# Optimization experiments

Hardware: AMD Instinct MI355X
Metric: run time of the kernel (lower is better)

## Reference

```python
import jax, jax.numpy as jnp
import numpy as np

IMG = 1024.0
NMS_THRESH = 0.7
PRE_NMS_TOPK = 1000
POST_NMS_TOPK = 1000
MIN_BOX_SIZE = 0.0
SCALE_CLAMP = float(np.log(1000.0 / 16.0))
NEG = -1e9
LVL_OFFSET = 2.0 * IMG  # batched_nms coordinate-offset trick: boxes from different levels never overlap

_STRIDES = [4, 8, 16, 32, 64]
_SIZES = [32.0, 64.0, 128.0, 256.0, 512.0]
_RATIOS = [0.5, 1.0, 2.0]


def _make_anchors():
    """Detectron2 DefaultAnchorGenerator anchors (offset=0)."""
    out = []
    for s, size in zip(_STRIDES, _SIZES):
        area = size * size
        base = []
        for r in _RATIOS:
            w = np.sqrt(area / r)
            h = r * w
            base.append([-w / 2.0, -h / 2.0, w / 2.0, h / 2.0])
        base = np.asarray(base, np.float32)  # [A,4]
        H = int(IMG) // s
        coords = np.arange(H, dtype=np.float32) * s
        sx, sy = np.meshgrid(coords, coords)
        shifts = np.stack([sx.ravel(), sy.ravel(), sx.ravel(), sy.ravel()], axis=1)  # [HW,4]
        anchors = (shifts[:, None, :] + base[None, :, :]).reshape(-1, 4).astype(np.float32)
        out.append(jnp.asarray(anchors))
    return out


def setup_inputs() -> dict:
    key = jax.random.key(0)
    N = 4
    names = ["p2", "p3", "p4", "p5", "p6"]
    anchors = _make_anchors()
    inp = {}
    for i, (nm, an) in enumerate(zip(names, anchors)):
        HWA = an.shape[0]
        k1 = jax.random.fold_in(key, 2 * i)
        k2 = jax.random.fold_in(key, 2 * i + 1)
        inp[f"logits_{nm}"] = jax.random.normal(k1, (N, HWA), jnp.float32)
        # small deltas so decoded proposals stay realistic
        inp[f"deltas_{nm}"] = 0.1 * jax.random.normal(k2, (N, HWA, 4), jnp.float32)
        inp[f"anchors_{nm}"] = an
    return inp


def _apply_deltas(deltas, anchors):
    """Box2BoxTransform.apply_deltas with weights (1,1,1,1)."""
    wa = anchors[..., 2] - anchors[..., 0]
    ha = anchors[..., 3] - anchors[..., 1]
    cxa = anchors[..., 0] + 0.5 * wa
    cya = anchors[..., 1] + 0.5 * ha
    dx, dy, dw, dh = (deltas[..., i] for i in range(4))
    dw = jnp.minimum(dw, SCALE_CLAMP)
    dh = jnp.minimum(dh, SCALE_CLAMP)
    cx = dx * wa + cxa
    cy = dy * ha + cya
    w = wa * jnp.exp(dw)
    h = ha * jnp.exp(dh)
    return jnp.stack([cx - 0.5 * w, cy - 0.5 * h, cx + 0.5 * w, cy + 0.5 * h], axis=-1)


def _pairwise_iou(b):
    area = (b[:, 2] - b[:, 0]) * (b[:, 3] - b[:, 1])
    lt = jnp.maximum(b[:, None, :2], b[None, :, :2])
    rb = jnp.minimum(b[:, None, 2:], b[None, :, 2:])
    wh = jnp.clip(rb - lt, 0.0)
    inter = wh[..., 0] * wh[..., 1]
    return inter / (area[:, None] + area[None, :] - inter + 1e-9)


def _nms_single(boxes, scores, lvl):
    """Greedy batched NMS (per-level via coordinate offset) + post-NMS top-k. boxes [M,4]."""
    M = boxes.shape[0]
    order = jnp.argsort(-scores)
    boxes = boxes[order]
    scores = scores[order]
    lvl = lvl[order]
    off_boxes = boxes + (lvl.astype(boxes.dtype) * LVL_OFFSET)[:, None]
    iou = _pairwise_iou(off_boxes)  # [M,M]
    valid = scores > NEG / 2
    idx = jnp.arange(M)

    def body(supp, xs):
        row, i, v = xs
        keep_i = (~supp[i]) & v
        supp = supp | (keep_i & (row > NMS_THRESH) & (idx > i))
        return supp, None

    supp, _ = jax.lax.scan(body, jnp.zeros((M,), bool), (iou, idx, valid))
    kept_scores = jnp.where((~supp) & valid, scores, NEG)
    top_s, top_i = jax.lax.top_k(kept_scores, POST_NMS_TOPK)
    return boxes[top_i], top_s


def _forward(logits_list, deltas_list, anchors_list):
    all_b, all_s, all_l = [], [], []
    for li, (lg, dl, an) in enumerate(zip(logits_list, deltas_list, anchors_list)):
        props = _apply_deltas(dl, an[None, :, :])  # [N,HWA,4]
        k = min(PRE_NMS_TOPK, lg.shape[1])
        sc, idx = jax.lax.top_k(lg, k)  # per-level pre-NMS top-k
        bx = jnp.take_along_axis(props, idx[..., None], axis=1)
        all_b.append(bx)
        all_s.append(sc)
        all_l.append(jnp.full((k,), li, jnp.int32))
    boxes = jnp.concatenate(all_b, axis=1)  # [N,M,4]
    scores = jnp.concatenate(all_s, axis=1)  # [N,M]
    lvl = jnp.concatenate(all_l, axis=0)  # [M]
    # clip to image + min-size filter (min_box_size = 0)
    boxes = jnp.clip(boxes, 0.0, IMG)
    w = boxes[..., 2] - boxes[..., 0]
    h = boxes[..., 3] - boxes[..., 1]
    scores = jnp.where((w > MIN_BOX_SIZE) & (h > MIN_BOX_SIZE), scores, NEG)
    return jax.vmap(_nms_single, in_axes=(0, 0, None))(boxes, scores, lvl)


def reference(logits_p2, logits_p3, logits_p4, logits_p5, logits_p6,
              deltas_p2, deltas_p3, deltas_p4, deltas_p5, deltas_p6,
              anchors_p2, anchors_p3, anchors_p4, anchors_p5, anchors_p6):
    logits = [logits_p2, logits_p3, logits_p4, logits_p5, logits_p6]
    deltas = [deltas_p2, deltas_p3, deltas_p4, deltas_p5, deltas_p6]
    anchors = [anchors_p2, anchors_p3, anchors_p4, anchors_p5, anchors_p6]
    boxes, scores = _forward(logits, deltas, anchors)
    return boxes, scores
```

## Files before the change

kernel.cpp:

```cpp
#include <hip/hip_runtime.h>
#include <stdint.h>
#include <math.h>

#define NLVL 5
#define NIMG 4
#define NGRP (NIMG * NLVL)
#define M_TOT 4768
#define POST_K 1000
#define NEGV  (-1e9f)
#define CAP 2048
#define BPI 65
#define TRI_W 7680
#define CNT_STRIDE 32
#define RD_SPLIT 8

__constant__ int c_hwa[NLVL]  = {196608, 49152, 12288, 3072, 768};
__constant__ int c_k[NLVL]    = {1000, 1000, 1000, 1000, 768};
__constant__ int c_base[NLVL] = {0, 1000, 2000, 3000, 4000};
__constant__ int c_cnt[NLVL]  = {4096, 4096, 4096, 3072, 768};
__constant__ uint32_t c_T0[NLVL] = {0xC019999Au, 0xBFECCCCDu, 0xBF933333u, 0x80000000u, 0x00000000u};

struct Ptrs {
    const float* logits[NLVL];
    const float* deltas[NLVL];
    const float* anchors[NLVL];
};

__device__ __forceinline__ uint32_t flipf(float f) {
    uint32_t b = __float_as_uint(f);
    return (b & 0x80000000u) ? ~b : (b | 0x80000000u);
}
__device__ __forceinline__ float unflipf(uint32_t key) {
    uint32_t b = (key & 0x80000000u) ? (key & 0x7FFFFFFFu) : ~key;
    return __uint_as_float(b);
}
__device__ __forceinline__ float rdlane_f(float v, int l) {
    return __uint_as_float((uint32_t)__builtin_amdgcn_readlane((int)__float_as_uint(v), l));
}

__device__ __forceinline__ void grp_decompose(int g, int& img, int& lvl, int& off, int& cnt) {
    img = g / BPI;
    int r = g % BPI;
    if (r < 48)      { lvl = 0; off = r * 4096; }
    else if (r < 60) { lvl = 1; off = (r - 48) * 4096; }
    else if (r < 63) { lvl = 2; off = (r - 60) * 4096; }
    else if (r < 64) { lvl = 3; off = 0; }
    else             { lvl = 4; off = 0; }
    cnt = c_cnt[lvl];
}

__device__ __forceinline__ uint32_t wave_or32(uint32_t v) {
    v |= (uint32_t)__builtin_amdgcn_update_dpp(0, (int)v, 0x111, 0xf, 0xf, true);
    v |= (uint32_t)__builtin_amdgcn_update_dpp(0, (int)v, 0x112, 0xf, 0xf, true);
    v |= (uint32_t)__builtin_amdgcn_update_dpp(0, (int)v, 0x114, 0xf, 0xf, true);
    v |= (uint32_t)__builtin_amdgcn_update_dpp(0, (int)v, 0x118, 0xf, 0xf, true);
    v |= (uint32_t)__builtin_amdgcn_update_dpp(0, (int)v, 0x142, 0xf, 0xf, true);
    v |= (uint32_t)__builtin_amdgcn_update_dpp(0, (int)v, 0x143, 0xf, 0xf, true);
    return (uint32_t)__builtin_amdgcn_readlane((int)v, 63);
}

__global__ void kCompactSpec(Ptrs p, uint32_t* __restrict__ cand_cnt,
                             uint64_t* __restrict__ cand_pk) {
    int img, lvl, off, cnt;
    grp_decompose(blockIdx.x, img, lvl, off, cnt);
    const int grp = img * NLVL + lvl;
    const int tid = threadIdx.x;
    const float* lg = p.logits[lvl] + (size_t)img * c_hwa[lvl] + off;
    const uint32_t T = c_T0[lvl];
    uint64_t* pk = cand_pk + (size_t)grp * CAP;

    __shared__ uint32_t scnt, sbase;
    __shared__ uint64_t sbuf[4096];
    if (tid == 0) scnt = 0u;
    __syncthreads();

    const int nvec = cnt >> 2;
    const float4* lg4 = (const float4*)lg;
    for (int v = tid; v < nvec; v += 256) {
        float4 x = lg4[v];
        float xs[4] = {x.x, x.y, x.z, x.w};
        #pragma unroll
        for (int c = 0; c < 4; ++c) {
            uint32_t key = flipf(xs[c]);
            if (key >= T) {
                uint32_t pos = atomicAdd(&scnt, 1u);
                uint32_t eidx = (uint32_t)(off + 4 * v + c);
                sbuf[pos] = ((uint64_t)key << 32) | (uint32_t)(~eidx);
            }
        }
    }
    __syncthreads();
    if (tid == 0) sbase = atomicAdd(&cand_cnt[grp * CNT_STRIDE], scnt);
    __syncthreads();
    const uint32_t n = scnt, b0 = sbase;
    for (uint32_t i = tid; i < n; i += 256) {
        uint32_t g = b0 + i;
        if (g < CAP) pk[g] = sbuf[i];
    }
}

__global__ void kFixup(Ptrs p, uint32_t* __restrict__ cand_cnt,
                       uint64_t* __restrict__ cand_pk) {
    const int grp = blockIdx.x;
    const int lvl = grp % NLVL;
    const int img = grp / NLVL;
    const int k = c_k[lvl];
    {
        uint32_t c = cand_cnt[grp * CNT_STRIDE];
        if (c >= (uint32_t)k && c <= CAP) return;
    }
    const int n = c_hwa[lvl];
    const float* lg = p.logits[lvl] + (size_t)img * n;
    const int tid = threadIdx.x, bs = blockDim.x;

    __shared__ uint32_t hist[256];
    __shared__ uint32_t sh_pre, sh_rem;
    if (tid == 0) { sh_pre = 0u; sh_rem = (uint32_t)k; cand_cnt[grp * CNT_STRIDE] = 0u; }

    for (int pass = 0; pass < 4; ++pass) {
        for (int i = tid; i < 256; i += bs) hist[i] = 0u;
        __syncthreads();
        const int shift = 24 - 8 * pass;
        const uint32_t pre = sh_pre;
        for (int i = tid; i < n; i += bs) {
            uint32_t key = flipf(lg[i]);
            if (pass == 0 || (key >> (shift + 8)) == pre)
                atomicAdd(&hist[(key >> shift) & 255u], 1u);
        }
        __syncthreads();
        if (tid == 0) {
            uint32_t rem = sh_rem;
            int d = 255;
            for (; d > 0; --d) {
                uint32_t c = hist[d];
                if (rem <= c) break;
                rem -= c;
            }
            sh_rem = rem;
            sh_pre = (pre << 8) | (uint32_t)d;
        }
        __syncthreads();
    }
    const uint32_t T = sh_pre;
    uint64_t* pk = cand_pk + (size_t)grp * CAP;
    for (int i = tid; i < n; i += bs) {
        uint32_t key = flipf(lg[i]);
        if (key >= T) {
            uint32_t pos = atomicAdd(&cand_cnt[grp * CNT_STRIDE], 1u);
            if (pos < CAP) pk[pos] = ((uint64_t)key << 32) | (uint32_t)(~(uint32_t)i);
        }
    }
}

__global__ void kRankDecode(Ptrs p, const uint32_t* __restrict__ cand_cnt,
                            const uint64_t* __restrict__ cand_pk,
                            float* __restrict__ cand_box,
                            float* __restrict__ cand_score) {
    #pragma clang fp contract(off)
    const int blk = blockIdx.x;
    const int grp = blk / RD_SPLIT;
    const int sub = blk % RD_SPLIT;
    const int img = grp / NLVL;
    const int lvl = grp % NLVL;
    const int n    = c_hwa[lvl];
    const int k    = c_k[lvl];
    const int base = c_base[lvl];
    const int tid = threadIdx.x;

    const int cc = (int)min(cand_cnt[grp * CNT_STRIDE], (uint32_t)CAP);
    const int c0 = sub * (CAP / RD_SPLIT);
    if (c0 >= cc) return;

    __shared__ uint64_t K[CAP];
    const uint64_t* pk = cand_pk + (size_t)grp * CAP;
    for (int i = tid; i < cc; i += 256) K[i] = pk[i];
    __syncthreads();

    const int c = c0 + tid;
    const uint64_t myK = (c < cc) ? K[c] : ~0ull;
    int r = 0;
    int j = 0;
    for (; j + 8 <= cc; j += 8) {
        #pragma unroll
        for (int u = 0; u < 8; ++u) r += (int)(K[j + u] > myK);
    }
    for (; j < cc; ++j) r += (int)(K[j] > myK);

    if (c >= cc || r >= k) return;

    uint32_t key = (uint32_t)(myK >> 32);
    uint32_t ic  = ~(uint32_t)(myK & 0xFFFFFFFFu);
    const float* an = p.anchors[lvl] + (size_t)ic * 4;
    const float* dl = p.deltas[lvl] + ((size_t)img * n + ic) * 4;
    float a0 = an[0], a1 = an[1], a2 = an[2], a3 = an[3];
    float wa = a2 - a0, ha = a3 - a1;
    float cxa = a0 + 0.5f * wa, cya = a1 + 0.5f * ha;
    float dx = dl[0], dy = dl[1], dw = dl[2], dh = dl[3];
    const float SC = (float)4.135166556742356;
    dw = fminf(dw, SC);
    dh = fminf(dh, SC);
    float cx = dx * wa + cxa, cy = dy * ha + cya;
    float w = wa * expf(dw), h = ha * expf(dh);
    float x1 = cx - 0.5f * w, y1 = cy - 0.5f * h;
    float x2 = cx + 0.5f * w, y2 = cy + 0.5f * h;
    x1 = fminf(fmaxf(x1, 0.0f), 1024.0f);
    y1 = fminf(fmaxf(y1, 0.0f), 1024.0f);
    x2 = fminf(fmaxf(x2, 0.0f), 1024.0f);
    y2 = fminf(fmaxf(y2, 0.0f), 1024.0f);
    float bw = x2 - x1, bh = y2 - y1;
    float score = (bw > 0.0f && bh > 0.0f) ? unflipf(key) : NEGV;
    const int slot = base + r;
    float* ob = cand_box + ((size_t)img * M_TOT + slot) * 4;
    ob[0] = x1; ob[1] = y1; ob[2] = x2; ob[3] = y2;
    cand_score[(size_t)img * M_TOT + slot] = score;
}

__global__ void kIou(const float* __restrict__ cand_box,
                     uint64_t* __restrict__ tri, uint64_t* __restrict__ diag) {
    #pragma clang fp contract(off)
    const int blk = blockIdx.x;
    const int grp = blk >> 6;
    const int w   = (blk >> 2) & 15;
    const int ch  = blk & 3;
    const int img = grp / NLVL;
    const int lvl = grp % NLVL;
    const int k    = c_k[lvl];
    const int base = c_base[lvl];
    if (64 * w >= k) return;
    const int R  = min(64 * (w + 1), k);
    const int r0 = ch * 256;
    if (r0 >= R) return;
    const int jn = min(64, k - 64 * w);
    const float lo = (float)lvl * 2048.0f;
    const int tid = threadIdx.x;
    const int lane = tid & 63;

    const int jl = (lane < jn) ? lane : 0;
    const float4 jb = *(const float4*)(cand_box + ((size_t)img * M_TOT + base + 64 * w + jl) * 4);
    const float jx1r = jb.x + lo, jy1r = jb.y + lo;
    const float jx2r = jb.z + lo, jy2r = jb.w + lo;
    const float jarr = (jx2r - jx1r) * (jy2r - jy1r);

    const int r = r0 + tid;
    const bool act = r < R;
    float rx1 = 0, ry1 = 0, rx2 = 0, ry2 = 0, ra = 0;
    if (act) {
        const float4 b = *(const float4*)(cand_box + ((size_t)img * M_TOT + base + r) * 4);
        rx1 = b.x + lo; ry1 = b.y + lo; rx2 = b.z + lo; ry2 = b.w + lo;
        ra = (rx2 - rx1) * (ry2 - ry1);
    }

    uint64_t bits = 0ull;
    #pragma unroll 4
    for (int jj = 0; jj < jn; ++jj) {
        const float bx1 = rdlane_f(jx1r, jj);
        const float by1 = rdlane_f(jy1r, jj);
        const float bx2 = rdlane_f(jx2r, jj);
        const float by2 = rdlane_f(jy2r, jj);
        const float bar = rdlane_f(jarr, jj);
        const int j = 64 * w + jj;
        if (j > r) {
            float ltx = fmaxf(rx1, bx1);
            float lty = fmaxf(ry1, by1);
            float rbx = fminf(rx2, bx2);
            float rby = fminf(ry2, by2);
            float wx = fmaxf(rbx - ltx, 0.0f);
            float wy = fmaxf(rby - lty, 0.0f);
            float inter = wx * wy;
            float denom = ((ra + bar) - inter) + 1e-9f;
            if (inter / denom > 0.7f) bits |= (1ull << jj);
        }
    }

    if (act) {
        if ((r >> 6) == w) diag[(size_t)grp * 1024 + r] = bits;
        else               tri[(size_t)grp * TRI_W + 32 * w * (w - 1) + r] = bits;
    }
}

__global__ void kScan(const float* __restrict__ cand_score,
                      const uint64_t* __restrict__ tri,
                      const uint64_t* __restrict__ diag,
                      uint32_t* __restrict__ kept) {
    const int grp = blockIdx.x;
    const int img = grp / NLVL;
    const int lvl = grp % NLVL;
    const int k    = c_k[lvl];
    const int base = c_base[lvl];
    const int lane = threadIdx.x;

    __shared__ uint64_t sdiag[1024];
    __shared__ uint64_t sinv[16];

    const uint64_t* dg_g = diag + (size_t)grp * 1024;
    #pragma unroll
    for (int s = 0; s < 16; ++s) {
        const int r = 64 * s + lane;
        uint64_t d = (r < k) ? dg_g[r] : 0ull;
        sdiag[r] = d;
        float sc = (r < k) ? cand_score[(size_t)img * M_TOT + base + r] : NEGV;
        uint64_t iv = __ballot(sc <= -5e8f);
        if (lane == 0) sinv[s] = iv;
    }
    __syncthreads();

    const uint64_t* trig = tri + (size_t)grp * TRI_W;
    uint32_t mykept = 0u;
    const int nstage = (k + 63) >> 6;

    #pragma unroll 1
    for (int q = 0; q < nstage; ++q) {
        const uint64_t* tq = trig + 32 * q * (q - 1);
        uint64_t vals[15];
        #pragma unroll
        for (int s = 0; s < 15; ++s)
            if (s < q) vals[s] = tq[64 * s + lane];
        uint64_t v = 0ull;
        #pragma unroll
        for (int s = 0; s < 15; ++s)
            if (s < q) {
                uint64_t msk = (uint64_t)0 - (uint64_t)((mykept >> s) & 1u);
                v |= vals[s] & msk;
            }
        const uint32_t vlo = wave_or32((uint32_t)v);
        const uint32_t vhi = wave_or32((uint32_t)(v >> 32));
        const uint64_t invq = sinv[q];
        const uint32_t ivlo = __builtin_amdgcn_readfirstlane((uint32_t)invq);
        const uint32_t ivhi = __builtin_amdgcn_readfirstlane((uint32_t)(invq >> 32));
        uint64_t rem = ~((((uint64_t)ivhi << 32) | (uint64_t)ivlo)
                       | (((uint64_t)vhi  << 32) | (uint64_t)vlo));

        const uint64_t darrq = sdiag[64 * q + lane];
        const uint32_t dlo = (uint32_t)darrq, dhi = (uint32_t)(darrq >> 32);
        const uint64_t nz = __ballot(darrq != 0ull);

        uint64_t kw = 0ull;
        for (;;) {
            uint64_t t = rem & nz;
            if (t == 0ull) { kw |= rem; break; }
            const int m = (int)__builtin_ctzll(t);
            const uint64_t bm = 1ull << m;
            const uint64_t lowm = bm - 1ull;
            kw |= (rem & lowm) | bm;
            const uint64_t dg =
                ((uint64_t)(uint32_t)__builtin_amdgcn_readlane((int)dhi, m) << 32)
              |  (uint64_t)(uint32_t)__builtin_amdgcn_readlane((int)dlo, m);
            rem &= ~(lowm | bm | dg);
        }
        mykept |= ((uint32_t)((kw >> lane) & 1ull)) << q;
    }

    #pragma unroll
    for (int s = 0; s < 16; ++s) {
        const int r = 64 * s + lane;
        if (r < k)
            kept[(size_t)img * M_TOT + base + r] = (mykept >> s) & 1u;
    }
}

__device__ __forceinline__ int bs_count_ge(const uint32_t* a, int n, uint32_t x) {
    int lo = 0, hi = n;
    while (lo < hi) { int mid = (lo + hi) >> 1; if (a[mid] >= x) lo = mid + 1; else hi = mid; }
    return lo;
}
__device__ __forceinline__ int bs_count_gt(const uint32_t* a, int n, uint32_t x) {
    int lo = 0, hi = n;
    while (lo < hi) { int mid = (lo + hi) >> 1; if (a[mid] > x) lo = mid + 1; else hi = mid; }
    return lo;
}

__global__ void kMergeOut(const float* __restrict__ cand_box,
                          const float* __restrict__ cand_score,
                          const uint32_t* __restrict__ kept,
                          float* __restrict__ out) {
    const int img = blockIdx.x;
    const int tid = threadIdx.x;
    const int lane = tid & 63, wave = tid >> 6;

    __shared__ uint32_t vkey[NLVL * 1024];
    __shared__ uint32_t ord[M_TOT];
    __shared__ uint32_t wsum[NLVL][16];
    __shared__ int wtot[16];

    uint32_t mykey[NLVL];
    int myvalid[NLVL], mylower[NLVL];
    #pragma unroll
    for (int L = 0; L < NLVL; ++L) {
        const int kL = c_k[L];
        const bool act = tid < kL;
        float s = act ? cand_score[(size_t)img * M_TOT + c_base[L] + tid] : NEGV;
        bool valid = act && (s > -5e8f);
        uint64_t mask = __ballot(valid);
        mylower[L] = (int)__popcll(mask & ((1ull << lane) - 1ull));
        if (lane == 0) wsum[L][wave] = (uint32_t)__popcll(mask);
        mykey[L] = flipf(s);
        myvalid[L] = valid ? 1 : 0;
    }
    __syncthreads();

    int nv[NLVL], myvpre[NLVL];
    #pragma unroll
    for (int L = 0; L < NLVL; ++L) {
        int pw = 0, tot = 0;
        #pragma unroll
        for (int w = 0; w < 16; ++w) {
            if (w < wave) pw += (int)wsum[L][w];
            tot += (int)wsum[L][w];
        }
        nv[L] = tot;
        myvpre[L] = pw + mylower[L];
        if (tid < c_k[L] && myvalid[L])
            vkey[L * 1024 + myvpre[L]] = mykey[L];
    }
    int totalValid = 0;
    #pragma unroll
    for (int L = 0; L < NLVL; ++L) totalValid += nv[L];
    __syncthreads();

    int invBase = totalValid;
    #pragma unroll
    for (int L = 0; L < NLVL; ++L) {
        const int kL = c_k[L];
        if (tid < kL) {
            const int slot = c_base[L] + tid;
            if (myvalid[L]) {
                const uint32_t x = mykey[L];
                int pos = myvpre[L];
                #pragma unroll
                for (int Lp = 0; Lp < NLVL; ++Lp) {
                    if (Lp == L) continue;
                    pos += (Lp < L) ? bs_count_ge(&vkey[Lp * 1024], nv[Lp], x)
                                    : bs_count_gt(&vkey[Lp * 1024], nv[Lp], x);
                }
                const uint32_t kp = kept[(size_t)img * M_TOT + slot];
                ord[pos] = (uint32_t)slot | (kp << 31);
            } else {
                const int inv_idx = tid - myvpre[L];
                ord[invBase + inv_idx] = (uint32_t)slot;
            }
        }
        invBase += (c_k[L] - nv[L]);
    }
    __syncthreads();

    const int PT = 5;
    const int pos0 = tid * PT;
    int flags[PT];
    uint32_t slots[PT];
    int lsum = 0;
    #pragma unroll
    for (int q = 0; q < PT; ++q) {
        int pp = pos0 + q;
        int kf = 0; uint32_t sl = 0;
        if (pp < M_TOT) {
            uint32_t o = ord[pp];
            sl = o & 0x7FFFFFFFu;
            kf = (int)(o >> 31);
        }
        flags[q] = kf; slots[q] = sl; lsum += kf;
    }
    int incl = lsum;
    #pragma unroll
    for (int off = 1; off < 64; off <<= 1) {
        int t = __shfl_up(incl, off, 64);
        if (lane >= off) incl += t;
    }
    if (lane == 63) wtot[wave] = incl;
    __syncthreads();
    int wpre = 0, total = 0;
    #pragma unroll
    for (int w = 0; w < 16; ++w) {
        int v = wtot[w];
        if (w < wave) wpre += v;
        total += v;
    }
    const int excl = wpre + (incl - lsum);

    int run = 0;
    #pragma unroll
    for (int q = 0; q < PT; ++q) {
        int pp = pos0 + q;
        if (pp >= M_TOT) break;
        int kf = flags[q];
        int kbefore = excl + run;
        run += kf;
        int oidx = kf ? kbefore : (total + (pp - kbefore));
        if (oidx < POST_K) {
            uint32_t sl = slots[q];
            const float4 b = *(const float4*)(cand_box + ((size_t)img * M_TOT + sl) * 4);
            float* ob = out + ((size_t)img * POST_K + oidx) * 4;
            ob[0] = b.x; ob[1] = b.y; ob[2] = b.z; ob[3] = b.w;
            out[NIMG * POST_K * 4 + (size_t)img * POST_K + oidx] =
                kf ? cand_score[(size_t)img * M_TOT + sl] : NEGV;
        }
    }
}

extern "C" void kernel_launch(void* const* d_in, const int* in_sizes, int n_in,
                              void* d_out, int out_size, void* d_ws, size_t ws_size,
                              hipStream_t stream) {
    Ptrs p;
    for (int l = 0; l < NLVL; ++l) {
        p.logits[l]  = (const float*)d_in[3 * l + 0];
        p.deltas[l]  = (const float*)d_in[3 * l + 1];
        p.anchors[l] = (const float*)d_in[3 * l + 2];
    }

    char* w = (char*)d_ws;
    float* cand_box   = (float*)w;        w += (size_t)NIMG * M_TOT * 4 * sizeof(float);
    float* cand_score = (float*)w;        w += (size_t)NIMG * M_TOT * sizeof(float);
    uint32_t* kept        = (uint32_t*)w; w += (size_t)NIMG * M_TOT * sizeof(uint32_t);
    uint64_t* cand_pk     = (uint64_t*)w; w += (size_t)NGRP * CAP * sizeof(uint64_t);
    uint64_t* tri         = (uint64_t*)w; w += (size_t)NGRP * TRI_W * sizeof(uint64_t);
    uint64_t* diag        = (uint64_t*)w; w += (size_t)NGRP * 1024 * sizeof(uint64_t);
    uint32_t* cand_cnt    = (uint32_t*)w; w += (size_t)NGRP * CNT_STRIDE * sizeof(uint32_t);

    hipMemsetAsync(cand_cnt, 0, (size_t)NGRP * CNT_STRIDE * sizeof(uint32_t), stream);

    kCompactSpec<<<NIMG * BPI,       256, 0, stream>>>(p, cand_cnt, cand_pk);
    kFixup      <<<NGRP,             256, 0, stream>>>(p, cand_cnt, cand_pk);
    kRankDecode <<<NGRP * RD_SPLIT,  256, 0, stream>>>(p, cand_cnt, cand_pk, cand_box, cand_score);
    kIou        <<<NGRP * 64,        256, 0, stream>>>(cand_box, tri, diag);
    kScan       <<<NGRP,              64, 0, stream>>>(cand_score, tri, diag, kept);
    kMergeOut   <<<NIMG,            1024, 0, stream>>>(cand_box, cand_score, kept, (float*)d_out);
}
```

Baseline: 192.3 us.

## Drop global atomics and fixup kernel; merge per-block candidate lists in rank kernel

Compaction blocks now write their candidates to private per-block slots with a per-block count, so the global atomic counters and the memset are no longer needed. The rank/decode kernel computes prefix offsets over the block counts, gathers the candidates by binary search, and runs the radix-select fallback inline when the speculative threshold gives too few or too many candidates. This removes two launches (the memset and kFixup) at the cost of a serial prefix loop per block and a fallback duplicated across the RD_SPLIT sub-blocks.

```diff
diff --git a/kernel.cpp b/kernel.cpp
--- a/kernel.cpp
+++ b/kernel.cpp
@@ -11,13 +11,15 @@
 #define CAP 2048
 #define BPI 65
 #define TRI_W 7680
-#define CNT_STRIDE 32
 #define RD_SPLIT 8
+#define UCAP 2048
 
 __constant__ int c_hwa[NLVL]  = {196608, 49152, 12288, 3072, 768};
 __constant__ int c_k[NLVL]    = {1000, 1000, 1000, 1000, 768};
 __constant__ int c_base[NLVL] = {0, 1000, 2000, 3000, 4000};
 __constant__ int c_cnt[NLVL]  = {4096, 4096, 4096, 3072, 768};
+__constant__ int c_us[NLVL]   = {0, 48, 60, 63, 64};
+__constant__ int c_un[NLVL]   = {48, 12, 3, 1, 1};
 __constant__ uint32_t c_T0[NLVL] = {0xC019999Au, 0xBFECCCCDu, 0xBF933333u, 0x80000000u, 0x00000000u};
 
 struct Ptrs {
@@ -59,17 +61,16 @@
     return (uint32_t)__builtin_amdgcn_readlane((int)v, 63);
 }
 
-__global__ void kCompactSpec(Ptrs p, uint32_t* __restrict__ cand_cnt,
-                             uint64_t* __restrict__ cand_pk) {
+__global__ void kCompactSpec(Ptrs p, uint32_t* __restrict__ ucnt,
+                             uint64_t* __restrict__ pk2) {
     int img, lvl, off, cnt;
-    grp_decompose(blockIdx.x, img, lvl, off, cnt);
-    const int grp = img * NLVL + lvl;
+    const int u = blockIdx.x;
+    grp_decompose(u, img, lvl, off, cnt);
     const int tid = threadIdx.x;
     const float* lg = p.logits[lvl] + (size_t)img * c_hwa[lvl] + off;
     const uint32_t T = c_T0[lvl];
-    uint64_t* pk = cand_pk + (size_t)grp * CAP;
-
-    __shared__ uint32_t scnt, sbase;
+
+    __shared__ uint32_t scnt;
     __shared__ uint64_t sbuf[4096];
     if (tid == 0) scnt = 0u;
     __syncthreads();
@@ -90,70 +91,15 @@
         }
     }
     __syncthreads();
-    if (tid == 0) sbase = atomicAdd(&cand_cnt[grp * CNT_STRIDE], scnt);
-    __syncthreads();
-    const uint32_t n = scnt, b0 = sbase;
-    for (uint32_t i = tid; i < n; i += 256) {
-        uint32_t g = b0 + i;
-        if (g < CAP) pk[g] = sbuf[i];
-    }
-}
-
-__global__ void kFixup(Ptrs p, uint32_t* __restrict__ cand_cnt,
-                       uint64_t* __restrict__ cand_pk) {
-    const int grp = blockIdx.x;
-    const int lvl = grp % NLVL;
-    const int img = grp / NLVL;
-    const int k = c_k[lvl];
-    {
-        uint32_t c = cand_cnt[grp * CNT_STRIDE];
-        if (c >= (uint32_t)k && c <= CAP) return;
-    }
-    const int n = c_hwa[lvl];
-    const float* lg = p.logits[lvl] + (size_t)img * n;
-    const int tid = threadIdx.x, bs = blockDim.x;
-
-    __shared__ uint32_t hist[256];
-    __shared__ uint32_t sh_pre, sh_rem;
-    if (tid == 0) { sh_pre = 0u; sh_rem = (uint32_t)k; cand_cnt[grp * CNT_STRIDE] = 0u; }
-
-    for (int pass = 0; pass < 4; ++pass) {
-        for (int i = tid; i < 256; i += bs) hist[i] = 0u;
-        __syncthreads();
-        const int shift = 24 - 8 * pass;
-        const uint32_t pre = sh_pre;
-        for (int i = tid; i < n; i += bs) {
-            uint32_t key = flipf(lg[i]);
-            if (pass == 0 || (key >> (shift + 8)) == pre)
-                atomicAdd(&hist[(key >> shift) & 255u], 1u);
-        }
-        __syncthreads();
-        if (tid == 0) {
-            uint32_t rem = sh_rem;
-            int d = 255;
-            for (; d > 0; --d) {
-                uint32_t c = hist[d];
-                if (rem <= c) break;
-                rem -= c;
-            }
-            sh_rem = rem;
-            sh_pre = (pre << 8) | (uint32_t)d;
-        }
-        __syncthreads();
-    }
-    const uint32_t T = sh_pre;
-    uint64_t* pk = cand_pk + (size_t)grp * CAP;
-    for (int i = tid; i < n; i += bs) {
-        uint32_t key = flipf(lg[i]);
-        if (key >= T) {
-            uint32_t pos = atomicAdd(&cand_cnt[grp * CNT_STRIDE], 1u);
-            if (pos < CAP) pk[pos] = ((uint64_t)key << 32) | (uint32_t)(~(uint32_t)i);
-        }
-    }
-}
-
-__global__ void kRankDecode(Ptrs p, const uint32_t* __restrict__ cand_cnt,
-                            const uint64_t* __restrict__ cand_pk,
+    const uint32_t n = scnt;
+    if (tid == 0) ucnt[u] = n;
+    const uint32_t nw = min(n, (uint32_t)UCAP);
+    uint64_t* pk = pk2 + (size_t)u * UCAP;
+    for (uint32_t i = tid; i < nw; i += 256) pk[i] = sbuf[i];
+}
+
+__global__ void kRankDecode(Ptrs p, const uint32_t* __restrict__ ucnt,
+                            const uint64_t* __restrict__ pk2,
                             float* __restrict__ cand_box,
                             float* __restrict__ cand_score) {
     #pragma clang fp contract(off)
@@ -166,15 +112,91 @@
     const int k    = c_k[lvl];
     const int base = c_base[lvl];
     const int tid = threadIdx.x;
-
-    const int cc = (int)min(cand_cnt[grp * CNT_STRIDE], (uint32_t)CAP);
-    const int c0 = sub * (CAP / RD_SPLIT);
-    if (c0 >= cc) return;
+    const int nu  = c_un[lvl];
+    const int u0  = img * BPI + c_us[lvl];
+    const int c0  = sub * (CAP / RD_SPLIT);
 
     __shared__ uint64_t K[CAP];
-    const uint64_t* pk = cand_pk + (size_t)grp * CAP;
-    for (int i = tid; i < cc; i += 256) K[i] = pk[i];
-    __syncthreads();
+    __shared__ int soff[49];
+    __shared__ uint32_t hist[256];
+    __shared__ uint32_t sh_pre, sh_rem, scnt2;
+    __shared__ int scc, sbad;
+
+    if (tid == 0) {
+        int o = 0, bad = 0;
+        for (int i = 0; i < nu; ++i) {
+            int c = (int)ucnt[u0 + i];
+            soff[i] = o;
+            if (c > UCAP) bad = 1;
+            o += c;
+        }
+        soff[nu] = o;
+        scc = o; sbad = bad;
+    }
+    __syncthreads();
+    int cc = scc;
+    const bool fb = sbad || (cc < k) || (cc > CAP);
+
+    if (!fb) {
+        if (c0 >= cc) return;
+        uint64_t vb[8];
+        int tt[8];
+        #pragma unroll
+        for (int q = 0; q < 8; ++q) {
+            const int t = tid + q * 256;
+            tt[q] = t;
+            if (t < cc) {
+                int lo2 = 0, hi2 = nu - 1;
+                while (lo2 < hi2) {
+                    int mid = (lo2 + hi2 + 1) >> 1;
+                    if (soff[mid] <= t) lo2 = mid; else hi2 = mid - 1;
+                }
+                vb[q] = pk2[(size_t)(u0 + lo2) * UCAP + (t - soff[lo2])];
+            }
+        }
+        #pragma unroll
+        for (int q = 0; q < 8; ++q)
+            if (tt[q] < cc) K[tt[q]] = vb[q];
+        __syncthreads();
+    } else {
+        const float* lg = p.logits[lvl] + (size_t)img * n;
+        if (tid == 0) { sh_pre = 0u; sh_rem = (uint32_t)k; scnt2 = 0u; }
+        for (int pass = 0; pass < 4; ++pass) {
+            hist[tid] = 0u;
+            __syncthreads();
+            const int shift = 24 - 8 * pass;
+            const uint32_t pre = sh_pre;
+            for (int i = tid; i < n; i += 256) {
+                uint32_t key = flipf(lg[i]);
+                if (pass == 0 || (key >> (shift + 8)) == pre)
+                    atomicAdd(&hist[(key >> shift) & 255u], 1u);
+            }
+            __syncthreads();
+            if (tid == 0) {
+                uint32_t rem = sh_rem;
+                int d = 255;
+                for (; d > 0; --d) {
+                    uint32_t c = hist[d];
+                    if (rem <= c) break;
+                    rem -= c;
+                }
+                sh_rem = rem;
+                sh_pre = (pre << 8) | (uint32_t)d;
+            }
+            __syncthreads();
+        }
+        const uint32_t T = sh_pre;
+        for (int i = tid; i < n; i += 256) {
+            uint32_t key = flipf(lg[i]);
+            if (key >= T) {
+                uint32_t pos = atomicAdd(&scnt2, 1u);
+                if (pos < CAP) K[pos] = ((uint64_t)key << 32) | (uint32_t)(~(uint32_t)i);
+            }
+        }
+        __syncthreads();
+        cc = (int)min(scnt2, (uint32_t)CAP);
+        if (c0 >= cc) return;
+    }
 
     const int c = c0 + tid;
     const uint64_t myK = (c < cc) ? K[c] : ~0ull;
@@ -510,16 +532,13 @@
     float* cand_box   = (float*)w;        w += (size_t)NIMG * M_TOT * 4 * sizeof(float);
     float* cand_score = (float*)w;        w += (size_t)NIMG * M_TOT * sizeof(float);
     uint32_t* kept        = (uint32_t*)w; w += (size_t)NIMG * M_TOT * sizeof(uint32_t);
-    uint64_t* cand_pk     = (uint64_t*)w; w += (size_t)NGRP * CAP * sizeof(uint64_t);
+    uint64_t* pk2         = (uint64_t*)w; w += (size_t)NIMG * BPI * UCAP * sizeof(uint64_t);
     uint64_t* tri         = (uint64_t*)w; w += (size_t)NGRP * TRI_W * sizeof(uint64_t);
     uint64_t* diag        = (uint64_t*)w; w += (size_t)NGRP * 1024 * sizeof(uint64_t);
-    uint32_t* cand_cnt    = (uint32_t*)w; w += (size_t)NGRP * CNT_STRIDE * sizeof(uint32_t);
-
-    hipMemsetAsync(cand_cnt, 0, (size_t)NGRP * CNT_STRIDE * sizeof(uint32_t), stream);
-
-    kCompactSpec<<<NIMG * BPI,       256, 0, stream>>>(p, cand_cnt, cand_pk);
-    kFixup      <<<NGRP,             256, 0, stream>>>(p, cand_cnt, cand_pk);
-    kRankDecode <<<NGRP * RD_SPLIT,  256, 0, stream>>>(p, cand_cnt, cand_pk, cand_box, cand_score);
+    uint32_t* ucnt        = (uint32_t*)w; w += (size_t)NIMG * BPI * sizeof(uint32_t);
+
+    kCompactSpec<<<NIMG * BPI,       256, 0, stream>>>(p, ucnt, pk2);
+    kRankDecode <<<NGRP * RD_SPLIT,  256, 0, stream>>>(p, ucnt, pk2, cand_box, cand_score);
     kIou        <<<NGRP * 64,        256, 0, stream>>>(cand_box, tri, diag);
     kScan       <<<NGRP,              64, 0, stream>>>(cand_score, tri, diag, kept);
     kMergeOut   <<<NIMG,            1024, 0, stream>>>(cand_box, cand_score, kept, (float*)d_out);
```

Result: faster. 185.4 us (-3.6%).
